# Optimization experiments

Hardware: AMD Instinct MI355X
Metric: run time of the kernel (lower is better)

The kernel has to match this reference:

```python
import jax, jax.numpy as jnp
import numpy as np

N_NODES = 100000
N_EDGES = 3200000
NFEAT = 256
HDIM = 64
NCLASS = 64
K = 4
ALPHA = 0.1


def setup_inputs() -> dict:
    key = jax.random.key(0)
    k1, k2, k3, k4, k5, k6 = jax.random.split(key, 6)
    x = jax.random.normal(k1, (N_NODES, NFEAT), dtype=jnp.float32)
    edge_index = jax.random.randint(k2, (2, N_EDGES), 0, N_NODES, dtype=jnp.int64)
    W_in = jax.random.normal(k3, (HDIM, NFEAT), dtype=jnp.float32) * (1.0 / np.sqrt(NFEAT))
    b_in = jax.random.normal(k4, (HDIM,), dtype=jnp.float32) * 0.01
    W_out = jax.random.normal(k5, (NCLASS, HDIM), dtype=jnp.float32) * (1.0 / np.sqrt(HDIM))
    b_out = jax.random.normal(k6, (NCLASS,), dtype=jnp.float32) * 0.01
    return {"x": x, "edge_index": edge_index, "W_in": W_in, "b_in": b_in,
            "W_out": W_out, "b_out": b_out}


def _gcn_norm(edge_index, n_nodes):
    # add self-loops, then symmetric normalization (PyG gcn_norm defaults)
    loops = jnp.arange(n_nodes, dtype=edge_index.dtype)
    src = jnp.concatenate([edge_index[0], loops])
    dst = jnp.concatenate([edge_index[1], loops])
    deg = jax.ops.segment_sum(jnp.ones_like(dst, dtype=jnp.float32), dst,
                              num_segments=n_nodes)
    dinv = jnp.where(deg > 0, 1.0 / jnp.sqrt(deg), 0.0)
    w = dinv[src] * dinv[dst]  # [E+N]
    return src, dst, w


def reference(x, edge_index, W_in, b_in, W_out, b_out):
    n = x.shape[0]
    src, dst, w = _gcn_norm(edge_index, n)
    h = x @ W_in.T + b_in                      # [N, 64]
    x0 = h
    for _ in range(K):                         # APPNP: (1-a) * A_hat h + a * x0
        agg = jax.ops.segment_sum(w[:, None] * h[src], dst, num_segments=n)
        h = (1.0 - ALPHA) * agg + ALPHA * x0
    h = jax.nn.relu(h)
    return h @ W_out.T + b_out                 # [N, nclass]
```

## Files before the change

### kernel.cpp

```cpp
#include <hip/hip_runtime.h>
#include <hip/hip_fp16.h>

#define NN 100000
#define NE 3200000
#define NFEAT 256
#define HDIM 64
#define NCLASS 64
#define ALPHA 0.1f
#define CAP 80

#define NB 256
#define BKN 391
#define EBLK (NE / 256)
#define BCAP 24
#define RCAP 96

typedef _Float16 half8 __attribute__((ext_vector_type(8)));
typedef float f32x4 __attribute__((ext_vector_type(4)));


__global__ __launch_bounds__(1024) void bucket_edges(const int* __restrict__ ei,
                                                     unsigned* __restrict__ pairs,
                                                     int* __restrict__ cntg) {
    __shared__ unsigned buf[NB][BCAP];
    __shared__ int cnt[NB];
    __shared__ int rcur[NB];
    int blk = blockIdx.x;
    int t = threadIdx.x;
    int e0 = blk * EBLK;
    for (int i = t; i < NB; i += 1024) { cnt[i] = 0; rcur[i] = 0; }
    __syncthreads();

    for (int eb = 0; eb < EBLK; eb += 1024) {
        bool act = (eb + t) < EBLK;
        if (act) {
            int e = e0 + eb + t;
            unsigned d = (unsigned)ei[NE + e];
            unsigned src = (unsigned)ei[e];
            unsigned b = d / BKN;
            unsigned w = (src << 9) | (d - b * BKN);
            int p = atomicAdd(&cnt[b], 1);
            if (p < BCAP) buf[b][p] = w;
        }
        __syncthreads();
        int lane = t & 63, wv = t >> 6;
        for (int j = 0; j < 16; j++) {
            int b2 = wv * 16 + j;
            int c = cnt[b2]; if (c > BCAP) c = BCAP;
            int rb = rcur[b2];
            if (lane < c) {
                int idx = rb + lane;
                if (idx < RCAP)
                    pairs[((size_t)blk * NB + b2) * RCAP + idx] = buf[b2][lane];
            }
            if (lane == 0) rcur[b2] = rb + c;
        }
        __syncthreads();
        if (t < NB) cnt[t] = 0;
        __syncthreads();
    }
    if (t < NB) cntg[blk * NB + t] = min(rcur[t], RCAP);
}


__global__ __launch_bounds__(1024) void fill_bucket(const unsigned* __restrict__ pairs,
                                                    const int* __restrict__ cntg,
                                                    int* __restrict__ col,
                                                    int* __restrict__ deg,
                                                    float* __restrict__ dinv) {
    __shared__ int cur[BKN];
    __shared__ int pref[NB + 1];
    __shared__ int cnts[NB];
    int b = blockIdx.x;
    int t = threadIdx.x;
    unsigned lo = (unsigned)b * BKN;
    for (int i = t; i < BKN; i += 1024) cur[i] = 0;
    if (t < NB) cnts[t] = cntg[t * NB + b];
    __syncthreads();
    if (t == 0) {
        int run = 0;
        for (int k = 0; k < NB; k++) { pref[k] = run; run += cnts[k]; }
        pref[NB] = run;
    }
    __syncthreads();
    int T = pref[NB];
    for (int i0 = 0; i0 < T; i0 += 1024) {
        int i = i0 + t;
        if (i < T) {
            int l = 0, h = NB;
            while (h - l > 1) { int m = (l + h) >> 1; if (pref[m] <= i) l = m; else h = m; }
            unsigned w = pairs[((size_t)l * NB + b) * RCAP + (i - pref[l])];
            unsigned dl = w & 511;
            unsigned src = w >> 9;
            int slot = atomicAdd(&cur[dl], 1);
            if (slot < CAP && lo + dl < NN)
                col[(size_t)(lo + dl) * CAP + slot] = (int)src;
        }
    }
    __syncthreads();
    for (int i = t; i < BKN; i += 1024) {
        unsigned node = lo + i;
        if (node < NN) {
            int dgv = cur[i];
            deg[node] = dgv;
            dinv[node] = rsqrtf((float)dgv + 1.f);
        }
    }
}


__global__ void prep_w(const float* __restrict__ W, _Float16* __restrict__ W2g) {
    int i = blockIdx.x * 256 + threadIdx.x;
    if (i >= 32 * 64) return;
    int kg = i >> 6;
    int n = i & 63;
    int slot = (kg << 6) + (n ^ ((kg & 3) << 2));
    _Float16 tmp[8];
#pragma unroll
    for (int j = 0; j < 8; j++) tmp[j] = (_Float16)W[n * 256 + kg * 8 + j];
    *(half8*)&W2g[(size_t)slot * 8] = *(half8*)tmp;
}


__global__ __launch_bounds__(256) void gemm1_mfma(const float* __restrict__ x,
                                                  const _Float16* __restrict__ W2g,
                                                  const float* __restrict__ bias,
                                                  const float* __restrict__ dinv,
                                                  _Float16* __restrict__ g0) {
    __shared__ _Float16 W2[32 * 64 * 8];
    int t = threadIdx.x;
    for (int i = t; i < 2048; i += 256)
        *(half8*)&W2[(size_t)i * 8] = *(const half8*)&W2g[(size_t)i * 8];
    __syncthreads();

    int lane = t & 63;
    int w = t >> 6;
    int r16 = lane & 15, kg = lane >> 4;
    int row0 = blockIdx.x * 128;
    int rowA = row0 + w * 32 + r16;
    int rowB = rowA + 16;
    int rA = rowA < NN ? rowA : NN - 1;
    int rB = rowB < NN ? rowB : NN - 1;
    const float* pa = &x[(size_t)rA * 256 + kg * 8];
    const float* pb = &x[(size_t)rB * 256 + kg * 8];

    f32x4 acc[2][4];
#pragma unroll
    for (int mt = 0; mt < 2; mt++)
#pragma unroll
        for (int nt = 0; nt < 4; nt++) acc[mt][nt] = (f32x4){0.f, 0.f, 0.f, 0.f};

#pragma unroll
    for (int ks = 0; ks < 8; ks++) {
        float4 va0 = *(const float4*)(pa + ks * 32);
        float4 va1 = *(const float4*)(pa + ks * 32 + 4);
        float4 vb0 = *(const float4*)(pb + ks * 32);
        float4 vb1 = *(const float4*)(pb + ks * 32 + 4);
        _Float16 a0h[8] = {(_Float16)va0.x, (_Float16)va0.y, (_Float16)va0.z, (_Float16)va0.w,
                           (_Float16)va1.x, (_Float16)va1.y, (_Float16)va1.z, (_Float16)va1.w};
        _Float16 a1h[8] = {(_Float16)vb0.x, (_Float16)vb0.y, (_Float16)vb0.z, (_Float16)vb0.w,
                           (_Float16)vb1.x, (_Float16)vb1.y, (_Float16)vb1.z, (_Float16)vb1.w};
        half8 a0 = *(half8*)a0h;
        half8 a1 = *(half8*)a1h;
        int kgg = ks * 4 + kg;
#pragma unroll
        for (int nt = 0; nt < 4; nt++) {
            int nidx = nt * 16 + r16;
            int slot = (kgg << 6) + (nidx ^ ((kgg & 3) << 2));
            half8 bfr = *(half8*)&W2[(size_t)slot * 8];
            acc[0][nt] = __builtin_amdgcn_mfma_f32_16x16x32_f16(a0, bfr, acc[0][nt], 0, 0, 0);
            acc[1][nt] = __builtin_amdgcn_mfma_f32_16x16x32_f16(a1, bfr, acc[1][nt], 0, 0, 0);
        }
    }

#pragma unroll
    for (int mt = 0; mt < 2; mt++)
#pragma unroll
        for (int nt = 0; nt < 4; nt++) {
            int colj = nt * 16 + r16;
            float bv = bias[colj];
#pragma unroll
            for (int r = 0; r < 4; r++) {
                int row = row0 + w * 32 + mt * 16 + kg * 4 + r;
                if (row < NN)
                    g0[(size_t)row * 64 + colj] = (_Float16)((acc[mt][nt][r] + bv) * dinv[row]);
            }
        }
}


template <int K, bool RELU>
__global__ __launch_bounds__(256) void gemm_nt(const float* __restrict__ A,
                                               const float* __restrict__ B,
                                               const float* __restrict__ bias,
                                               float* __restrict__ C, int M) {
    __shared__ float aT[32][132];
    __shared__ float bT[32][68];
    int t = threadIdx.x;
    int row0 = blockIdx.x * 128;
    int nq = t & 15;
    int jq = t >> 4;
    float acc[8][4];
#pragma unroll
    for (int i = 0; i < 8; i++)
#pragma unroll
        for (int c = 0; c < 4; c++) acc[i][c] = 0.f;

    for (int k0 = 0; k0 < K; k0 += 32) {
#pragma unroll
        for (int i = 0; i < 4; i++) {
            int id = t + i * 256;
            int n = id >> 3, kc = id & 7;
            int row = row0 + n;
            float4 v = make_float4(0.f, 0.f, 0.f, 0.f);
            if (row < M) v = *(const float4*)&A[(size_t)row * K + k0 + kc * 4];
            if (RELU) {
                v.x = fmaxf(v.x, 0.f); v.y = fmaxf(v.y, 0.f);
                v.z = fmaxf(v.z, 0.f); v.w = fmaxf(v.w, 0.f);
            }
            aT[kc * 4 + 0][n] = v.x; aT[kc * 4 + 1][n] = v.y;
            aT[kc * 4 + 2][n] = v.z; aT[kc * 4 + 3][n] = v.w;
        }
#pragma unroll
        for (int i = 0; i < 2; i++) {
            int id = t + i * 256;
            int j = id >> 3, kc = id & 7;
            float4 v = *(const float4*)&B[(size_t)j * K + k0 + kc * 4];
            bT[kc * 4 + 0][j] = v.x; bT[kc * 4 + 1][j] = v.y;
            bT[kc * 4 + 2][j] = v.z; bT[kc * 4 + 3][j] = v.w;
        }
        __syncthreads();
#pragma unroll
        for (int k = 0; k < 32; k++) {
            float4 a0 = *(const float4*)&aT[k][nq * 4];
            float4 a1 = *(const float4*)&aT[k][nq * 4 + 64];
            float4 b  = *(const float4*)&bT[k][jq * 4];
            float av[8] = {a0.x, a0.y, a0.z, a0.w, a1.x, a1.y, a1.z, a1.w};
            float bv[4] = {b.x, b.y, b.z, b.w};
#pragma unroll
            for (int i = 0; i < 8; i++)
#pragma unroll
                for (int c = 0; c < 4; c++) acc[i][c] += av[i] * bv[c];
        }
        __syncthreads();
    }

    float4 b4 = *(const float4*)&bias[jq * 4];
#pragma unroll
    for (int i = 0; i < 8; i++) {
        int row = row0 + ((i < 4) ? (nq * 4 + i) : (64 + nq * 4 + (i - 4)));
        if (row < M) {
            float4 o;
            o.x = acc[i][0] + b4.x; o.y = acc[i][1] + b4.y;
            o.z = acc[i][2] + b4.z; o.w = acc[i][3] + b4.w;
            *(float4*)&C[(size_t)row * 64 + jq * 4] = o;
        }
    }
}


__device__ inline void acc8(float4 raw, float m, float acc[8]) {
    const __half2* h2 = (const __half2*)&raw;
#pragma unroll
    for (int j = 0; j < 4; j++) {
        float2 f = __half22float2(h2[j]);
        acc[2 * j]     = fmaf(m, f.x, acc[2 * j]);
        acc[2 * j + 1] = fmaf(m, f.y, acc[2 * j + 1]);
    }
}

template <bool FINAL>
__global__ __launch_bounds__(256) void appnp_prop_f(const __half* __restrict__ gcur,
                                                    void* __restrict__ gnext,
                                                    const __half* __restrict__ g0,
                                                    const float* __restrict__ dinv,
                                                    const int* __restrict__ deg,
                                                    const int* __restrict__ col) {
    int wid = (blockIdx.x * 256 + threadIdx.x) >> 6;
    int lane = threadIdx.x & 63;
    if (wid >= NN) return;
    int eg = lane >> 3;
    int q  = lane & 7;
    const float4* gc4 = (const float4*)gcur;

    float acc[8];
#pragma unroll
    for (int j = 0; j < 8; j++) acc[j] = 0.f;

    int dg = deg[wid]; if (dg > CAP) dg = CAP;
    int e0 = wid * CAP;
    int end = e0 + dg;
    int p = e0;
    for (; p + 8 < end; p += 16) {
        int i0 = p + eg, i1 = p + 8 + eg;
        float m1 = (i1 < end) ? 1.f : 0.f;
        int s0 = col[i0];
        int s1 = col[(i1 < end) ? i1 : end - 1];
        float4 r0 = gc4[(size_t)s0 * 8 + q];
        float4 r1 = gc4[(size_t)s1 * 8 + q];
        acc8(r0, 1.f, acc);
        acc8(r1, m1, acc);
    }
    if (p < end) {
        int i0 = p + eg;
        float m0 = (i0 < end) ? 1.f : 0.f;
        int s0 = col[(i0 < end) ? i0 : end - 1];
        float4 r0 = gc4[(size_t)s0 * 8 + q];
        acc8(r0, m0, acc);
    }

#pragma unroll
    for (int st = 8; st < 64; st <<= 1) {
#pragma unroll
        for (int j = 0; j < 8; j++) acc[j] += __shfl(acc[j], lane ^ st);
    }

    if (eg == 0) {
        float di = dinv[wid];
        float k = (1.f - ALPHA) * di * di;
        float4 sraw = gc4[(size_t)wid * 8 + q];
        float4 zraw = ((const float4*)g0)[(size_t)wid * 8 + q];
        const __half2* sh = (const __half2*)&sraw;
        const __half2* zh = (const __half2*)&zraw;
        float g[8];
#pragma unroll
        for (int j = 0; j < 4; j++) {
            float2 sf = __half22float2(sh[j]);
            float2 zf = __half22float2(zh[j]);
            g[2 * j]     = k * (acc[2 * j]     + sf.x) + ALPHA * zf.x;
            g[2 * j + 1] = k * (acc[2 * j + 1] + sf.y) + ALPHA * zf.y;
        }
        if (FINAL) {
            float inv = 1.f / di;
            float* ho = (float*)gnext;
            float4 o0 = make_float4(g[0] * inv, g[1] * inv, g[2] * inv, g[3] * inv);
            float4 o1 = make_float4(g[4] * inv, g[5] * inv, g[6] * inv, g[7] * inv);
            *(float4*)&ho[(size_t)wid * 64 + q * 8]     = o0;
            *(float4*)&ho[(size_t)wid * 64 + q * 8 + 4] = o1;
        } else {
            __half2 h2o[4];
#pragma unroll
            for (int j = 0; j < 4; j++) h2o[j] = __floats2half2_rn(g[2 * j], g[2 * j + 1]);
            *(float4*)&((__half*)gnext)[(size_t)wid * 64 + q * 8] = *(float4*)h2o;
        }
    }
}


extern "C" void kernel_launch(void* const* d_in, const int* in_sizes, int n_in,
                              void* d_out, int out_size, void* d_ws, size_t ws_size,
                              hipStream_t stream) {
    const float* x    = (const float*)d_in[0];
    const int*  ei    = (const int*)d_in[1];
    const float* W_in = (const float*)d_in[2];
    const float* b_in = (const float*)d_in[3];
    const float* W_out= (const float*)d_in[4];
    const float* b_out= (const float*)d_in[5];
    float* out = (float*)d_out;

    char* ws = (char*)d_ws;
    size_t off = 0;
    auto alloc = [&](size_t bytes) -> void* {
        void* p = ws + off;
        off = (off + bytes + 255) & ~(size_t)255;
        return p;
    };
    int*      deg  = (int*)    alloc((size_t)NN * 4);
    float*    dinv = (float*)  alloc((size_t)NN * 4);
    int*      cntg = (int*)    alloc((size_t)NB * 256 * 4);
    _Float16* W2g  = (_Float16*)alloc((size_t)32 * 64 * 8 * 2);
    int*      col  = (int*)    alloc((size_t)NN * CAP * 4);
    __half*   g0h  = (__half*) alloc((size_t)NN * HDIM * 2);
    __half*   gA   = (__half*) alloc((size_t)NN * HDIM * 2);
    __half*   gB   = (__half*) alloc((size_t)NN * HDIM * 2);
    unsigned* pairs = (unsigned*)g0h;

    bucket_edges<<<256, 1024, 0, stream>>>(ei, pairs, cntg);
    fill_bucket<<<NB, 1024, 0, stream>>>(pairs, cntg, col, deg, dinv);

    prep_w<<<8, 256, 0, stream>>>(W_in, W2g);
    gemm1_mfma<<<(NN + 127) / 128, 256, 0, stream>>>(x, W2g, b_in, dinv, (_Float16*)g0h);

    const int pgrid = (NN * HDIM) / 256;
    appnp_prop_f<false><<<pgrid, 256, 0, stream>>>(g0h, gA, g0h, dinv, deg, col);
    appnp_prop_f<false><<<pgrid, 256, 0, stream>>>(gA, gB, g0h, dinv, deg, col);
    appnp_prop_f<false><<<pgrid, 256, 0, stream>>>(gB, gA, g0h, dinv, deg, col);
    appnp_prop_f<true ><<<pgrid, 256, 0, stream>>>(gA, out, g0h, dinv, deg, col);

    gemm_nt<HDIM, true><<<(NN + 127) / 128, 256, 0, stream>>>(out, W_out, b_out, out, NN);
}
```

Baseline: 330.5 us.

## Use MFMA fp16 for output GEMM and half2 accumulation in propagation

Replaces the scalar fp32 output GEMM with an MFMA fp16 kernel that reuses the swizzled weight prep for W_out, applying ReLU and the fp16 conversion on load. The propagation kernel now accumulates neighbour sums and does its shuffle reduction in packed half2 instead of fp32, which halves the ALU work and the shuffle count. This trades accuracy: fp16 sums over up to 80 neighbours may lose precision or overflow.

```diff
diff --git a/kernel.cpp b/kernel.cpp
--- a/kernel.cpp
+++ b/kernel.cpp
@@ -109,15 +109,16 @@
 }
 
 
-__global__ void prep_w(const float* __restrict__ W, _Float16* __restrict__ W2g) {
+__global__ void prep_w(const float* __restrict__ W, _Float16* __restrict__ W2g,
+                       int KG, int Kfull) {
     int i = blockIdx.x * 256 + threadIdx.x;
-    if (i >= 32 * 64) return;
+    if (i >= KG * 64) return;
     int kg = i >> 6;
     int n = i & 63;
     int slot = (kg << 6) + (n ^ ((kg & 3) << 2));
     _Float16 tmp[8];
 #pragma unroll
-    for (int j = 0; j < 8; j++) tmp[j] = (_Float16)W[n * 256 + kg * 8 + j];
+    for (int j = 0; j < 8; j++) tmp[j] = (_Float16)W[n * Kfull + kg * 8 + j];
     *(half8*)&W2g[(size_t)slot * 8] = *(half8*)tmp;
 }
 
@@ -189,93 +190,83 @@
 }
 
 
-template <int K, bool RELU>
-__global__ __launch_bounds__(256) void gemm_nt(const float* __restrict__ A,
-                                               const float* __restrict__ B,
-                                               const float* __restrict__ bias,
-                                               float* __restrict__ C, int M) {
-    __shared__ float aT[32][132];
-    __shared__ float bT[32][68];
+__global__ __launch_bounds__(256) void gemm2_mfma(const float* __restrict__ h,
+                                                  const _Float16* __restrict__ W2o,
+                                                  const float* __restrict__ bias,
+                                                  float* __restrict__ out) {
+    __shared__ _Float16 W2[8 * 64 * 8];
     int t = threadIdx.x;
+    for (int i = t; i < 512; i += 256)
+        *(half8*)&W2[(size_t)i * 8] = *(const half8*)&W2o[(size_t)i * 8];
+    __syncthreads();
+
+    int lane = t & 63;
+    int w = t >> 6;
+    int r16 = lane & 15, kg = lane >> 4;
     int row0 = blockIdx.x * 128;
-    int nq = t & 15;
-    int jq = t >> 4;
-    float acc[8][4];
-#pragma unroll
-    for (int i = 0; i < 8; i++)
-#pragma unroll
-        for (int c = 0; c < 4; c++) acc[i][c] = 0.f;
-
-    for (int k0 = 0; k0 < K; k0 += 32) {
-#pragma unroll
-        for (int i = 0; i < 4; i++) {
-            int id = t + i * 256;
-            int n = id >> 3, kc = id & 7;
-            int row = row0 + n;
-            float4 v = make_float4(0.f, 0.f, 0.f, 0.f);
-            if (row < M) v = *(const float4*)&A[(size_t)row * K + k0 + kc * 4];
-            if (RELU) {
-                v.x = fmaxf(v.x, 0.f); v.y = fmaxf(v.y, 0.f);
-                v.z = fmaxf(v.z, 0.f); v.w = fmaxf(v.w, 0.f);
+    int rowA = row0 + w * 32 + r16;
+    int rowB = rowA + 16;
+    int rA = rowA < NN ? rowA : NN - 1;
+    int rB = rowB < NN ? rowB : NN - 1;
+    const float* pa = &h[(size_t)rA * 64 + kg * 8];
+    const float* pb = &h[(size_t)rB * 64 + kg * 8];
+
+    f32x4 acc[2][4];
+#pragma unroll
+    for (int mt = 0; mt < 2; mt++)
+#pragma unroll
+        for (int nt = 0; nt < 4; nt++) acc[mt][nt] = (f32x4){0.f, 0.f, 0.f, 0.f};
+
+#pragma unroll
+    for (int ks = 0; ks < 2; ks++) {
+        float4 va0 = *(const float4*)(pa + ks * 32);
+        float4 va1 = *(const float4*)(pa + ks * 32 + 4);
+        float4 vb0 = *(const float4*)(pb + ks * 32);
+        float4 vb1 = *(const float4*)(pb + ks * 32 + 4);
+        _Float16 a0h[8] = {(_Float16)fmaxf(va0.x, 0.f), (_Float16)fmaxf(va0.y, 0.f),
+                           (_Float16)fmaxf(va0.z, 0.f), (_Float16)fmaxf(va0.w, 0.f),
+                           (_Float16)fmaxf(va1.x, 0.f), (_Float16)fmaxf(va1.y, 0.f),
+                           (_Float16)fmaxf(va1.z, 0.f), (_Float16)fmaxf(va1.w, 0.f)};
+        _Float16 a1h[8] = {(_Float16)fmaxf(vb0.x, 0.f), (_Float16)fmaxf(vb0.y, 0.f),
+                           (_Float16)fmaxf(vb0.z, 0.f), (_Float16)fmaxf(vb0.w, 0.f),
+                           (_Float16)fmaxf(vb1.x, 0.f), (_Float16)fmaxf(vb1.y, 0.f),
+                           (_Float16)fmaxf(vb1.z, 0.f), (_Float16)fmaxf(vb1.w, 0.f)};
+        half8 a0 = *(half8*)a0h;
+        half8 a1 = *(half8*)a1h;
+        int kgg = ks * 4 + kg;
+#pragma unroll
+        for (int nt = 0; nt < 4; nt++) {
+            int nidx = nt * 16 + r16;
+            int slot = (kgg << 6) + (nidx ^ ((kgg & 3) << 2));
+            half8 bfr = *(half8*)&W2[(size_t)slot * 8];
+            acc[0][nt] = __builtin_amdgcn_mfma_f32_16x16x32_f16(a0, bfr, acc[0][nt], 0, 0, 0);
+            acc[1][nt] = __builtin_amdgcn_mfma_f32_16x16x32_f16(a1, bfr, acc[1][nt], 0, 0, 0);
+        }
+    }
+
+#pragma unroll
+    for (int mt = 0; mt < 2; mt++)
+#pragma unroll
+        for (int nt = 0; nt < 4; nt++) {
+            int colj = nt * 16 + r16;
+            float bv = bias[colj];
+#pragma unroll
+            for (int r = 0; r < 4; r++) {
+                int row = row0 + w * 32 + mt * 16 + kg * 4 + r;
+                if (row < NN)
+                    out[(size_t)row * 64 + colj] = acc[mt][nt][r] + bv;
             }
-            aT[kc * 4 + 0][n] = v.x; aT[kc * 4 + 1][n] = v.y;
-            aT[kc * 4 + 2][n] = v.z; aT[kc * 4 + 3][n] = v.w;
-        }
-#pragma unroll
-        for (int i = 0; i < 2; i++) {
-            int id = t + i * 256;
-            int j = id >> 3, kc = id & 7;
-            float4 v = *(const float4*)&B[(size_t)j * K + k0 + kc * 4];
-            bT[kc * 4 + 0][j] = v.x; bT[kc * 4 + 1][j] = v.y;
-            bT[kc * 4 + 2][j] = v.z; bT[kc * 4 + 3][j] = v.w;
-        }
-        __syncthreads();
-#pragma unroll
-        for (int k = 0; k < 32; k++) {
-            float4 a0 = *(const float4*)&aT[k][nq * 4];
-            float4 a1 = *(const float4*)&aT[k][nq * 4 + 64];
-            float4 b  = *(const float4*)&bT[k][jq * 4];
-            float av[8] = {a0.x, a0.y, a0.z, a0.w, a1.x, a1.y, a1.z, a1.w};
-            float bv[4] = {b.x, b.y, b.z, b.w};
-#pragma unroll
-            for (int i = 0; i < 8; i++)
-#pragma unroll
-                for (int c = 0; c < 4; c++) acc[i][c] += av[i] * bv[c];
-        }
-        __syncthreads();
-    }
-
-    float4 b4 = *(const float4*)&bias[jq * 4];
-#pragma unroll
-    for (int i = 0; i < 8; i++) {
-        int row = row0 + ((i < 4) ? (nq * 4 + i) : (64 + nq * 4 + (i - 4)));
-        if (row < M) {
-            float4 o;
-            o.x = acc[i][0] + b4.x; o.y = acc[i][1] + b4.y;
-            o.z = acc[i][2] + b4.z; o.w = acc[i][3] + b4.w;
-            *(float4*)&C[(size_t)row * 64 + jq * 4] = o;
-        }
-    }
-}
-
-
-__device__ inline void acc8(float4 raw, float m, float acc[8]) {
-    const __half2* h2 = (const __half2*)&raw;
-#pragma unroll
-    for (int j = 0; j < 4; j++) {
-        float2 f = __half22float2(h2[j]);
-        acc[2 * j]     = fmaf(m, f.x, acc[2 * j]);
-        acc[2 * j + 1] = fmaf(m, f.y, acc[2 * j + 1]);
-    }
-}
+        }
+}
+
 
 template <bool FINAL>
-__global__ __launch_bounds__(256) void appnp_prop_f(const __half* __restrict__ gcur,
-                                                    void* __restrict__ gnext,
-                                                    const __half* __restrict__ g0,
-                                                    const float* __restrict__ dinv,
-                                                    const int* __restrict__ deg,
-                                                    const int* __restrict__ col) {
+__global__ __launch_bounds__(256) void appnp_prop_h2(const __half* __restrict__ gcur,
+                                                     void* __restrict__ gnext,
+                                                     const __half* __restrict__ g0,
+                                                     const float* __restrict__ dinv,
+                                                     const int* __restrict__ deg,
+                                                     const int* __restrict__ col) {
     int wid = (blockIdx.x * 256 + threadIdx.x) >> 6;
     int lane = threadIdx.x & 63;
     if (wid >= NN) return;
@@ -283,9 +274,10 @@
     int q  = lane & 7;
     const float4* gc4 = (const float4*)gcur;
 
-    float acc[8];
-#pragma unroll
-    for (int j = 0; j < 8; j++) acc[j] = 0.f;
+    const __half2 hz = __floats2half2_rn(0.f, 0.f);
+    __half2 acc[4];
+#pragma unroll
+    for (int j = 0; j < 4; j++) acc[j] = hz;
 
     int dg = deg[wid]; if (dg > CAP) dg = CAP;
     int e0 = wid * CAP;
@@ -293,26 +285,37 @@
     int p = e0;
     for (; p + 8 < end; p += 16) {
         int i0 = p + eg, i1 = p + 8 + eg;
-        float m1 = (i1 < end) ? 1.f : 0.f;
+        bool ok1 = i1 < end;
         int s0 = col[i0];
-        int s1 = col[(i1 < end) ? i1 : end - 1];
+        int s1 = col[ok1 ? i1 : end - 1];
         float4 r0 = gc4[(size_t)s0 * 8 + q];
         float4 r1 = gc4[(size_t)s1 * 8 + q];
-        acc8(r0, 1.f, acc);
-        acc8(r1, m1, acc);
+        const __half2* v0 = (const __half2*)&r0;
+        const __half2* v1 = (const __half2*)&r1;
+#pragma unroll
+        for (int j = 0; j < 4; j++) {
+            acc[j] = __hadd2(acc[j], v0[j]);
+            acc[j] = __hadd2(acc[j], ok1 ? v1[j] : hz);
+        }
     }
     if (p < end) {
         int i0 = p + eg;
-        float m0 = (i0 < end) ? 1.f : 0.f;
-        int s0 = col[(i0 < end) ? i0 : end - 1];
+        bool ok0 = i0 < end;
+        int s0 = col[ok0 ? i0 : end - 1];
         float4 r0 = gc4[(size_t)s0 * 8 + q];
-        acc8(r0, m0, acc);
+        const __half2* v0 = (const __half2*)&r0;
+#pragma unroll
+        for (int j = 0; j < 4; j++)
+            acc[j] = __hadd2(acc[j], ok0 ? v0[j] : hz);
     }
 
 #pragma unroll
     for (int st = 8; st < 64; st <<= 1) {
 #pragma unroll
-        for (int j = 0; j < 8; j++) acc[j] += __shfl(acc[j], lane ^ st);
+        for (int j = 0; j < 4; j++) {
+            int o = __shfl(*(int*)&acc[j], lane ^ st);
+            acc[j] = __hadd2(acc[j], *(__half2*)&o);
+        }
     }
 
     if (eg == 0) {
@@ -325,10 +328,11 @@
         float g[8];
 #pragma unroll
         for (int j = 0; j < 4; j++) {
+            float2 a  = __half22float2(acc[j]);
             float2 sf = __half22float2(sh[j]);
             float2 zf = __half22float2(zh[j]);
-            g[2 * j]     = k * (acc[2 * j]     + sf.x) + ALPHA * zf.x;
-            g[2 * j + 1] = k * (acc[2 * j + 1] + sf.y) + ALPHA * zf.y;
+            g[2 * j]     = k * (a.x + sf.x) + ALPHA * zf.x;
+            g[2 * j + 1] = k * (a.y + sf.y) + ALPHA * zf.y;
         }
         if (FINAL) {
             float inv = 1.f / di;
@@ -369,6 +373,7 @@
     float*    dinv = (float*)  alloc((size_t)NN * 4);
     int*      cntg = (int*)    alloc((size_t)NB * 256 * 4);
     _Float16* W2g  = (_Float16*)alloc((size_t)32 * 64 * 8 * 2);
+    _Float16* W2o  = (_Float16*)alloc((size_t)8 * 64 * 8 * 2);
     int*      col  = (int*)    alloc((size_t)NN * CAP * 4);
     __half*   g0h  = (__half*) alloc((size_t)NN * HDIM * 2);
     __half*   gA   = (__half*) alloc((size_t)NN * HDIM * 2);
@@ -378,14 +383,16 @@
     bucket_edges<<<256, 1024, 0, stream>>>(ei, pairs, cntg);
     fill_bucket<<<NB, 1024, 0, stream>>>(pairs, cntg, col, deg, dinv);
 
-    prep_w<<<8, 256, 0, stream>>>(W_in, W2g);
+    prep_w<<<8, 256, 0, stream>>>(W_in, W2g, 32, 256);
+    prep_w<<<2, 256, 0, stream>>>(W_out, W2o, 8, 64);
+
     gemm1_mfma<<<(NN + 127) / 128, 256, 0, stream>>>(x, W2g, b_in, dinv, (_Float16*)g0h);
 
     const int pgrid = (NN * HDIM) / 256;
-    appnp_prop_f<false><<<pgrid, 256, 0, stream>>>(g0h, gA, g0h, dinv, deg, col);
-    appnp_prop_f<false><<<pgrid, 256, 0, stream>>>(gA, gB, g0h, dinv, deg, col);
-    appnp_prop_f<false><<<pgrid, 256, 0, stream>>>(gB, gA, g0h, dinv, deg, col);
-    appnp_prop_f<true ><<<pgrid, 256, 0, stream>>>(gA, out, g0h, dinv, deg, col);
-
-    gemm_nt<HDIM, true><<<(NN + 127) / 128, 256, 0, stream>>>(out, W_out, b_out, out, NN);
-}
+    appnp_prop_h2<false><<<pgrid, 256, 0, stream>>>(g0h, gA, g0h, dinv, deg, col);
+    appnp_prop_h2<false><<<pgrid, 256, 0, stream>>>(gA, gB, g0h, dinv, deg, col);
+    appnp_prop_h2<false><<<pgrid, 256, 0, stream>>>(gB, gA, g0h, dinv, deg, col);
+    appnp_prop_h2<true ><<<pgrid, 256, 0, stream>>>(gA, out, g0h, dinv, deg, col);
+
+    gemm2_mfma<<<(NN + 127) / 128, 256, 0, stream>>>(out, W2o, b_out, out);
+}
```

New measurement: 340.3 us. 1.03x slower.
